# Kernel tuning notes

Hardware: AMD Instinct MI355X
Metric: run time of the kernel (lower is better)

Reference implementation:

```python
import jax, jax.numpy as jnp
import numpy as np


def setup_inputs() -> dict:
    key = jax.random.key(0)
    ks = jax.random.split(key, 7)
    B, S, E, H, D = 4, 2048, 1024, 16, 64
    return {
        "q": jax.random.normal(ks[0], (B, S, E), dtype=jnp.float32),
        "k": jax.random.normal(ks[1], (B, S, E), dtype=jnp.float32),
        "v": jax.random.normal(ks[2], (B, S, E), dtype=jnp.float32),
        "Wq": jax.random.uniform(ks[3], (H, E, D), dtype=jnp.float32),
        "Wk": jax.random.uniform(ks[4], (H, E, D), dtype=jnp.float32),
        "Wv": jax.random.uniform(ks[5], (H, E, D), dtype=jnp.float32),
        "Wo": jax.random.uniform(ks[6], (H * D, E), dtype=jnp.float32),
    }


def reference(q, k, v, Wq, Wk, Wv, Wo):
    B, S, E = q.shape
    H, _, D = Wq.shape
    qh = jnp.einsum("bse,hed->bhsd", q, Wq)
    kh = jnp.einsum("bse,hed->bhsd", k, Wk)
    vh = jnp.einsum("bse,hed->bhsd", v, Wv)
    # Faithful quirk: original divides by C**(-0.5) -> multiplies by sqrt(D)
    scale = jnp.asarray(D, q.dtype) ** 0.5
    scores = jnp.einsum("bhsd,bhtd->bhst", qh, kh) * scale  # [B,H,S,S]
    causal = jnp.tril(jnp.ones((S, S), dtype=bool))
    scores = jnp.where(causal, scores, -jnp.inf)
    attn = jax.nn.softmax(scores, axis=-1)
    out_h = jnp.einsum("bhst,bhtd->bhsd", attn, vh)  # [B,H,S,D]
    concat = out_h.transpose(0, 2, 1, 3).reshape(B, S, H * D)
    return concat @ Wo
```

## Files before the change

### kernel.cpp

```cpp
#include <hip/hip_runtime.h>
#include <hip/hip_bf16.h>

#define B_ 4
#define S_ 2048
#define E_ 1024
#define H_ 16
#define D_ 64
#define LDW 40

typedef _Float16 f16;
typedef __attribute__((ext_vector_type(4))) float f32x4;
typedef __attribute__((ext_vector_type(8))) short bf16x8;
typedef __attribute__((ext_vector_type(8))) unsigned short u16x8;
typedef __attribute__((ext_vector_type(8))) _Float16 f16x8;
typedef __attribute__((ext_vector_type(4))) float float4v;

__device__ __forceinline__ unsigned short f2bf(float f) {
  union { float f; unsigned int u; } x; x.f = f;
  unsigned int u = x.u;
  u = (u + 0x7FFFu + ((u >> 16) & 1u)) >> 16;
  return (unsigned short)u;
}

#define MFMA_BF(a, b, c) __builtin_amdgcn_mfma_f32_16x16x32_bf16((a), (b), (c), 0, 0, 0)
#define MFMA_F16(a, b, c) __builtin_amdgcn_mfma_f32_16x16x32_f16((a), (b), (c), 0, 0, 0)

__global__ __launch_bounds__(256)
void transpose_convert(const float* __restrict__ src, unsigned short* __restrict__ dst,
                       int R, int C, float scale) {
  __shared__ unsigned short tile[64][65];
  const int rb = blockIdx.y * 64;
  const int cb = blockIdx.x * 64;
  const size_t mo = (size_t)blockIdx.z * (size_t)R * (size_t)C;
  const int t = threadIdx.x;
  const int r = t >> 2;
  const int c0 = (t & 3) * 16;
  const float* sp = src + mo + (size_t)(rb + r) * C + cb + c0;
#pragma unroll
  for (int j = 0; j < 16; j += 4) {
    float4v vv = *(const float4v*)(sp + j);
    tile[r][c0 + j + 0] = f2bf(vv[0] * scale);
    tile[r][c0 + j + 1] = f2bf(vv[1] * scale);
    tile[r][c0 + j + 2] = f2bf(vv[2] * scale);
    tile[r][c0 + j + 3] = f2bf(vv[3] * scale);
  }
  __syncthreads();
  u16x8 w0, w1;
#pragma unroll
  for (int j = 0; j < 8; ++j) w0[j] = tile[c0 + j][r];
#pragma unroll
  for (int j = 0; j < 8; ++j) w1[j] = tile[c0 + 8 + j][r];
  unsigned short* dp = dst + mo + (size_t)(cb + r) * R + rb + c0;
  *(u16x8*)(dp) = w0;
  *(u16x8*)(dp + 8) = w1;
}

__global__ __launch_bounds__(256)
void transpose_split_f16(const float* __restrict__ src, f16* __restrict__ dhi,
                         f16* __restrict__ dlo, int R, int C, float scale) {
  __shared__ float tile[64][65];
  const int rb = blockIdx.y * 64;
  const int cb = blockIdx.x * 64;
  const size_t mo = (size_t)blockIdx.z * (size_t)R * (size_t)C;
  const int t = threadIdx.x;
  const int r = t >> 2;
  const int c0 = (t & 3) * 16;
  const float* sp = src + mo + (size_t)(rb + r) * C + cb + c0;
#pragma unroll
  for (int j = 0; j < 16; j += 4) {
    float4v vv = *(const float4v*)(sp + j);
    tile[r][c0 + j + 0] = vv[0] * scale;
    tile[r][c0 + j + 1] = vv[1] * scale;
    tile[r][c0 + j + 2] = vv[2] * scale;
    tile[r][c0 + j + 3] = vv[3] * scale;
  }
  __syncthreads();
  f16x8 h0, h1, l0, l1;
#pragma unroll
  for (int j = 0; j < 8; ++j) {
    float x = tile[c0 + j][r];
    f16 hi = (f16)x;
    h0[j] = hi; l0[j] = (f16)(x - (float)hi);
  }
#pragma unroll
  for (int j = 0; j < 8; ++j) {
    float x = tile[c0 + 8 + j][r];
    f16 hi = (f16)x;
    h1[j] = hi; l1[j] = (f16)(x - (float)hi);
  }
  const size_t o = mo + (size_t)(cb + r) * R + rb + c0;
  *(f16x8*)(dhi + o) = h0; *(f16x8*)(dhi + o + 8) = h1;
  *(f16x8*)(dlo + o) = l0; *(f16x8*)(dlo + o + 8) = l1;
}

__global__ __launch_bounds__(256)
void prep_split(const float* __restrict__ x, f16* __restrict__ xh, f16* __restrict__ xl) {
  const size_t i = ((size_t)blockIdx.x * 256 + threadIdx.x) * 8;
  float4v a = *(const float4v*)(x + i);
  float4v b = *(const float4v*)(x + i + 4);
  f16x8 h, lo;
#pragma unroll
  for (int j = 0; j < 4; ++j) {
    f16 hi = (f16)a[j]; h[j] = hi; lo[j] = (f16)(a[j] - (float)hi);
  }
#pragma unroll
  for (int j = 0; j < 4; ++j) {
    f16 hi = (f16)b[j]; h[4 + j] = hi; lo[4 + j] = (f16)(b[j] - (float)hi);
  }
  *(f16x8*)(xh + i) = h;
  *(f16x8*)(xl + i) = lo;
}

__global__ __launch_bounds__(256)
void prep_bf16(const float* __restrict__ x, unsigned short* __restrict__ xo) {
  const size_t i = ((size_t)blockIdx.x * 256 + threadIdx.x) * 8;
  float4v a = *(const float4v*)(x + i);
  float4v b = *(const float4v*)(x + i + 4);
  u16x8 o;
#pragma unroll
  for (int j = 0; j < 4; ++j) { o[j] = f2bf(a[j]); o[4 + j] = f2bf(b[j]); }
  *(u16x8*)(xo + i) = o;
}

__global__ __launch_bounds__(256, 2)
void proj_qk2(const f16* __restrict__ xh, const f16* __restrict__ xl,
              const f16* __restrict__ Wh, const f16* __restrict__ Wl,
              f16* __restrict__ out_hi, f16* __restrict__ out_lo) {
  __shared__ f16 Ah[128 * LDW], Al[128 * LDW], Bh[128 * LDW], Bl[128 * LDW];
  const int t = threadIdx.x;
  const int m0 = blockIdx.x * 128, n0 = blockIdx.y * 128;
  const int w = t >> 6, l = t & 63, lr = l & 15, lg = l >> 4;
  const int wm = (w & 1) * 64, wn = (w >> 1) * 64;

  const int sr0 = t >> 2, sc = (t & 3) * 8;
  const f16* gAh = xh + (size_t)(m0 + sr0) * 1024 + sc;
  const f16* gAl = xl + (size_t)(m0 + sr0) * 1024 + sc;
  const f16* gBh = Wh + (size_t)(n0 + sr0) * 1024 + sc;
  const f16* gBl = Wl + (size_t)(n0 + sr0) * 1024 + sc;
  const size_t rstep = (size_t)64 * 1024;
  const int l0 = sr0 * LDW + sc, l1 = (sr0 + 64) * LDW + sc;

  f32x4 acc[4][4];
#pragma unroll
  for (int im = 0; im < 4; ++im)
#pragma unroll
    for (int in = 0; in < 4; ++in) acc[im][in] = (f32x4){0.f, 0.f, 0.f, 0.f};

  f16x8 r0 = *(const f16x8*)(gAh),         r1 = *(const f16x8*)(gAh + rstep);
  f16x8 r2 = *(const f16x8*)(gAl),         r3 = *(const f16x8*)(gAl + rstep);
  f16x8 r4 = *(const f16x8*)(gBh),         r5 = *(const f16x8*)(gBh + rstep);
  f16x8 r6 = *(const f16x8*)(gBl),         r7 = *(const f16x8*)(gBl + rstep);
  *(f16x8*)&Ah[l0] = r0; *(f16x8*)&Ah[l1] = r1;
  *(f16x8*)&Al[l0] = r2; *(f16x8*)&Al[l1] = r3;
  *(f16x8*)&Bh[l0] = r4; *(f16x8*)&Bh[l1] = r5;
  *(f16x8*)&Bl[l0] = r6; *(f16x8*)&Bl[l1] = r7;

  for (int k0 = 0; k0 < 1024; k0 += 32) {
    __syncthreads();
    const bool pf = (k0 + 32 < 1024);
    if (pf) {
      r0 = *(const f16x8*)(gAh + k0 + 32); r1 = *(const f16x8*)(gAh + rstep + k0 + 32);
      r2 = *(const f16x8*)(gAl + k0 + 32); r3 = *(const f16x8*)(gAl + rstep + k0 + 32);
      r4 = *(const f16x8*)(gBh + k0 + 32); r5 = *(const f16x8*)(gBh + rstep + k0 + 32);
      r6 = *(const f16x8*)(gBl + k0 + 32); r7 = *(const f16x8*)(gBl + rstep + k0 + 32);
    }
    f16x8 afh[4], afl[4], bfh[4], bfl[4];
#pragma unroll
    for (int im = 0; im < 4; ++im) {
      afh[im] = *(const f16x8*)&Ah[(wm + im * 16 + lr) * LDW + lg * 8];
      afl[im] = *(const f16x8*)&Al[(wm + im * 16 + lr) * LDW + lg * 8];
    }
#pragma unroll
    for (int in = 0; in < 4; ++in) {
      bfh[in] = *(const f16x8*)&Bh[(wn + in * 16 + lr) * LDW + lg * 8];
      bfl[in] = *(const f16x8*)&Bl[(wn + in * 16 + lr) * LDW + lg * 8];
    }
#pragma unroll
    for (int im = 0; im < 4; ++im)
#pragma unroll
      for (int in = 0; in < 4; ++in) {
        acc[im][in] = MFMA_F16(afh[im], bfh[in], acc[im][in]);
        acc[im][in] = MFMA_F16(afh[im], bfl[in], acc[im][in]);
        acc[im][in] = MFMA_F16(afl[im], bfh[in], acc[im][in]);
      }
    __syncthreads();
    if (pf) {
      *(f16x8*)&Ah[l0] = r0; *(f16x8*)&Ah[l1] = r1;
      *(f16x8*)&Al[l0] = r2; *(f16x8*)&Al[l1] = r3;
      *(f16x8*)&Bh[l0] = r4; *(f16x8*)&Bh[l1] = r5;
      *(f16x8*)&Bl[l0] = r6; *(f16x8*)&Bl[l1] = r7;
    }
  }

  const int b = m0 >> 11, s0b = m0 & 2047;
#pragma unroll
  for (int im = 0; im < 4; ++im)
#pragma unroll
    for (int in = 0; in < 4; ++in)
#pragma unroll
      for (int rr = 0; rr < 4; ++rr) {
        const int srow = s0b + wm + im * 16 + lg * 4 + rr;
        const int n = n0 + wn + in * 16 + lr;
        const int h = n >> 6, d = n & 63;
        const size_t o = (((size_t)b * H_ + h) * S_ + srow) * D_ + d;
        const float x = acc[im][in][rr];
        const f16 hi = (f16)x;
        out_hi[o] = hi;
        out_lo[o] = (f16)(x - (float)hi);
      }
}

__global__ __launch_bounds__(256, 2)
void proj_v2(const unsigned short* __restrict__ xv, const unsigned short* __restrict__ Wv,
             f16* __restrict__ vht) {
  __shared__ short smem[17408];
  unsigned short* As = (unsigned short*)smem;
  unsigned short* Bs = As + 128 * LDW;
  const int t = threadIdx.x;
  const int m0 = blockIdx.x * 128, n0 = blockIdx.y * 128;
  const int w = t >> 6, l = t & 63, lr = l & 15, lg = l >> 4;
  const int wm = (w & 1) * 64, wn = (w >> 1) * 64;

  const int sr0 = t >> 2, sc = (t & 3) * 8;
  const unsigned short* gA = xv + (size_t)(m0 + sr0) * 1024 + sc;
  const unsigned short* gB = Wv + (size_t)(n0 + sr0) * 1024 + sc;
  const size_t rstep = (size_t)64 * 1024;
  const int l0 = sr0 * LDW + sc, l1 = (sr0 + 64) * LDW + sc;

  f32x4 acc[4][4];
#pragma unroll
  for (int im = 0; im < 4; ++im)
#pragma unroll
    for (int in = 0; in < 4; ++in) acc[im][in] = (f32x4){0.f, 0.f, 0.f, 0.f};

  u16x8 r0 = *(const u16x8*)(gA), r1 = *(const u16x8*)(gA + rstep);
  u16x8 r2 = *(const u16x8*)(gB), r3 = *(const u16x8*)(gB + rstep);
  *(u16x8*)&As[l0] = r0; *(u16x8*)&As[l1] = r1;
  *(u16x8*)&Bs[l0] = r2; *(u16x8*)&Bs[l1] = r3;

  for (int k0 = 0; k0 < 1024; k0 += 32) {
    __syncthreads();
    const bool pf = (k0 + 32 < 1024);
    if (pf) {
      r0 = *(const u16x8*)(gA + k0 + 32); r1 = *(const u16x8*)(gA + rstep + k0 + 32);
      r2 = *(const u16x8*)(gB + k0 + 32); r3 = *(const u16x8*)(gB + rstep + k0 + 32);
    }
    bf16x8 af[4], bf[4];
#pragma unroll
    for (int im = 0; im < 4; ++im)
      af[im] = *(const bf16x8*)&As[(wm + im * 16 + lr) * LDW + lg * 8];
#pragma unroll
    for (int in = 0; in < 4; ++in)
      bf[in] = *(const bf16x8*)&Bs[(wn + in * 16 + lr) * LDW + lg * 8];
#pragma unroll
    for (int im = 0; im < 4; ++im)
#pragma unroll
      for (int in = 0; in < 4; ++in)
        acc[im][in] = MFMA_BF(af[im], bf[in], acc[im][in]);
    __syncthreads();
    if (pf) {
      *(u16x8*)&As[l0] = r0; *(u16x8*)&As[l1] = r1;
      *(u16x8*)&Bs[l0] = r2; *(u16x8*)&Bs[l1] = r3;
    }
  }

  __syncthreads();
  f16* Td = (f16*)smem;
#pragma unroll
  for (int im = 0; im < 4; ++im)
#pragma unroll
    for (int in = 0; in < 4; ++in)
#pragma unroll
      for (int rr = 0; rr < 4; ++rr) {
        const int srow = wm + im * 16 + lg * 4 + rr;
        const int ncol = wn + in * 16 + lr;
        Td[ncol * 136 + srow] = (f16)acc[im][in][rr];
      }
  __syncthreads();
  const int n = t >> 1, sc2 = (t & 1) * 64;
  const int b = m0 >> 11, s0b = m0 & 2047;
  const int h = (n0 + n) >> 6, d = (n0 + n) & 63;
  f16* vp = vht + (((size_t)b * H_ + h) * D_ + d) * S_ + s0b + sc2;
#pragma unroll
  for (int j = 0; j < 8; ++j)
    *(f16x8*)(vp + j * 8) = *(const f16x8*)&Td[n * 136 + sc2 + j * 8];
}

__global__ __launch_bounds__(256, 2)
void out_gemm2(const unsigned short* __restrict__ A, const unsigned short* __restrict__ Bt,
               float* __restrict__ Cout) {
  __shared__ unsigned short As[128 * LDW], Bs[128 * LDW];
  const int t = threadIdx.x;
  const int m0 = blockIdx.x * 128, n0 = blockIdx.y * 128;
  const int w = t >> 6, l = t & 63, lr = l & 15, lg = l >> 4;
  const int wm = (w & 1) * 64, wn = (w >> 1) * 64;

  const int sr0 = t >> 2, sc = (t & 3) * 8;
  const unsigned short* gA = A + (size_t)(m0 + sr0) * 1024 + sc;
  const unsigned short* gB = Bt + (size_t)(n0 + sr0) * 1024 + sc;
  const size_t rstep = (size_t)64 * 1024;
  const int l0 = sr0 * LDW + sc, l1 = (sr0 + 64) * LDW + sc;

  f32x4 acc[4][4];
#pragma unroll
  for (int im = 0; im < 4; ++im)
#pragma unroll
    for (int in = 0; in < 4; ++in) acc[im][in] = (f32x4){0.f, 0.f, 0.f, 0.f};

  u16x8 r0 = *(const u16x8*)(gA), r1 = *(const u16x8*)(gA + rstep);
  u16x8 r2 = *(const u16x8*)(gB), r3 = *(const u16x8*)(gB + rstep);
  *(u16x8*)&As[l0] = r0; *(u16x8*)&As[l1] = r1;
  *(u16x8*)&Bs[l0] = r2; *(u16x8*)&Bs[l1] = r3;

  for (int k0 = 0; k0 < 1024; k0 += 32) {
    __syncthreads();
    const bool pf = (k0 + 32 < 1024);
    if (pf) {
      r0 = *(const u16x8*)(gA + k0 + 32); r1 = *(const u16x8*)(gA + rstep + k0 + 32);
      r2 = *(const u16x8*)(gB + k0 + 32); r3 = *(const u16x8*)(gB + rstep + k0 + 32);
    }
    bf16x8 af[4], bf[4];
#pragma unroll
    for (int im = 0; im < 4; ++im)
      af[im] = *(const bf16x8*)&As[(wm + im * 16 + lr) * LDW + lg * 8];
#pragma unroll
    for (int in = 0; in < 4; ++in)
      bf[in] = *(const bf16x8*)&Bs[(wn + in * 16 + lr) * LDW + lg * 8];
#pragma unroll
    for (int im = 0; im < 4; ++im)
#pragma unroll
      for (int in = 0; in < 4; ++in)
        acc[im][in] = MFMA_BF(af[im], bf[in], acc[im][in]);
    __syncthreads();
    if (pf) {
      *(u16x8*)&As[l0] = r0; *(u16x8*)&As[l1] = r1;
      *(u16x8*)&Bs[l0] = r2; *(u16x8*)&Bs[l1] = r3;
    }
  }

#pragma unroll
  for (int im = 0; im < 4; ++im)
#pragma unroll
    for (int in = 0; in < 4; ++in)
#pragma unroll
      for (int rr = 0; rr < 4; ++rr) {
        const int row = m0 + wm + im * 16 + lg * 4 + rr;
        const int col = n0 + wn + in * 16 + lr;
        Cout[(size_t)row * 1024 + col] = acc[im][in][rr];
      }
}

__global__ __launch_bounds__(256, 2)
void attn_kernel(const f16* __restrict__ qhh, const f16* __restrict__ qhl,
                 const f16* __restrict__ khh, const f16* __restrict__ khl,
                 const f16* __restrict__ vht, unsigned short* __restrict__ ao) {
  __shared__ f16 Ksh[2][64 * 64];
  __shared__ f16 Ksl[2][64 * 64];
  __shared__ f16 Vts[2][64 * 64];
  __shared__ f16 Pls[4][32 * 64];
  const int t = threadIdx.x;
  const int b = blockIdx.z, h = blockIdx.y;
  const int w = t >> 6, l = t & 63, lr = l & 15, lg = l >> 4;
  const size_t bh = ((size_t)b * H_ + h) * S_;
  const size_t bhD = ((size_t)b * H_ + h) * D_;
  const int cr0 = t >> 3, cch = t & 7;
  const int cr1 = (t + 256) >> 3;
  const int coff = (cch * 16);

#pragma unroll
  for (int ph = 0; ph < 2; ++ph) {
    const int qt = ph ? (15 - (int)blockIdx.x) : (int)blockIdx.x;
    const int q0 = qt * 128;

    f16x8 qfh[2][2], qfl[2][2];
#pragma unroll
    for (int i = 0; i < 2; ++i) {
      const size_t qo = (bh + q0 + w * 32 + i * 16 + lr) * D_;
#pragma unroll
      for (int hf = 0; hf < 2; ++hf) {
        qfh[i][hf] = *(const f16x8*)(qhh + qo + hf * 32 + lg * 8);
        qfl[i][hf] = *(const f16x8*)(qhl + qo + hf * 32 + lg * 8);
      }
    }

    f32x4 acc[2][4];
#pragma unroll
    for (int i = 0; i < 2; ++i)
#pragma unroll
      for (int c = 0; c < 4; ++c) acc[i][c] = (f32x4){0.f, 0.f, 0.f, 0.f};
    float mx[2][4], ls[2][4];
#pragma unroll
    for (int i = 0; i < 2; ++i)
#pragma unroll
      for (int r = 0; r < 4; ++r) { mx[i][r] = -3.0e38f; ls[i][r] = 0.f; }

    const int wmax = q0 + w * 32 + 31;
    const int nkt = 2 * qt + 2;
    int cur = 0;

    {
      const f16* kbh = khh + bh * D_;
      const f16* kbl = khl + bh * D_;
      const f16* vb = vht + bhD * S_;
      f16x8 a0 = *(const f16x8*)(kbh + cr0 * 64 + cch * 8);
      f16x8 a1 = *(const f16x8*)(kbh + cr1 * 64 + cch * 8);
      f16x8 b0 = *(const f16x8*)(kbl + cr0 * 64 + cch * 8);
      f16x8 b1 = *(const f16x8*)(kbl + cr1 * 64 + cch * 8);
      f16x8 c0 = *(const f16x8*)(vb + (size_t)cr0 * S_ + cch * 8);
      f16x8 c1 = *(const f16x8*)(vb + (size_t)cr1 * S_ + cch * 8);
      const int o0 = coff ^ ((cr0 & 7) << 4);
      const int o1 = coff ^ ((cr1 & 7) << 4);
      *(f16x8*)((char*)Ksh[0] + cr0 * 128 + o0) = a0;
      *(f16x8*)((char*)Ksh[0] + cr1 * 128 + o1) = a1;
      *(f16x8*)((char*)Ksl[0] + cr0 * 128 + o0) = b0;
      *(f16x8*)((char*)Ksl[0] + cr1 * 128 + o1) = b1;
      *(f16x8*)((char*)Vts[0] + cr0 * 128 + o0) = c0;
      *(f16x8*)((char*)Vts[0] + cr1 * 128 + o1) = c1;
    }

    for (int kt = 0; kt < nkt; ++kt) {
      const int kt0 = kt * 64;
      __syncthreads();

      const bool pf = (kt + 1 < nkt);
      f16x8 ra0, ra1, rb0, rb1, rc0, rc1;
      if (pf) {
        const int n0 = kt0 + 64;
        const f16* kbh = khh + (bh + n0) * D_;
        const f16* kbl = khl + (bh + n0) * D_;
        const f16* vb = vht + bhD * S_ + n0;
        ra0 = *(const f16x8*)(kbh + cr0 * 64 + cch * 8);
        ra1 = *(const f16x8*)(kbh + cr1 * 64 + cch * 8);
        rb0 = *(const f16x8*)(kbl + cr0 * 64 + cch * 8);
        rb1 = *(const f16x8*)(kbl + cr1 * 64 + cch * 8);
        rc0 = *(const f16x8*)(vb + (size_t)cr0 * S_ + cch * 8);
        rc1 = *(const f16x8*)(vb + (size_t)cr1 * S_ + cch * 8);
      }

      if (kt0 <= wmax) {
        f32x4 sc[2][4];
#pragma unroll
        for (int n = 0; n < 4; ++n) {
          const int krow = n * 16 + lr;
          const int sw = (krow & 7) << 4;
          const char* kb = (const char*)Ksh[cur] + krow * 128;
          const char* kbl2 = (const char*)Ksl[cur] + krow * 128;
          f16x8 kh0 = *(const f16x8*)(kb + ((lg * 16) ^ sw));
          f16x8 kh1 = *(const f16x8*)(kb + ((64 + lg * 16) ^ sw));
          f16x8 kl0 = *(const f16x8*)(kbl2 + ((lg * 16) ^ sw));
          f16x8 kl1 = *(const f16x8*)(kbl2 + ((64 + lg * 16) ^ sw));
#pragma unroll
          for (int i = 0; i < 2; ++i) {
            f32x4 z = (f32x4){0.f, 0.f, 0.f, 0.f};
            z = MFMA_F16(qfh[i][0], kh0, z);
            z = MFMA_F16(qfh[i][1], kh1, z);
            z = MFMA_F16(qfh[i][0], kl0, z);
            z = MFMA_F16(qfh[i][1], kl1, z);
            z = MFMA_F16(qfl[i][0], kh0, z);
            z = MFMA_F16(qfl[i][1], kh1, z);
            sc[i][n] = z;
          }
        }

#pragma unroll
        for (int i = 0; i < 2; ++i) {
          const int qbase = q0 + w * 32 + i * 16;
          const bool full = (kt0 + 63 <= qbase);
#pragma unroll
          for (int r = 0; r < 4; ++r) {
            const int qrow = qbase + lg * 4 + r;
            float v0 = sc[i][0][r], v1 = sc[i][1][r], v2 = sc[i][2][r], v3 = sc[i][3][r];
            if (!full) {
              v0 = (kt0 + 0 + lr <= qrow) ? v0 : -3.0e38f;
              v1 = (kt0 + 16 + lr <= qrow) ? v1 : -3.0e38f;
              v2 = (kt0 + 32 + lr <= qrow) ? v2 : -3.0e38f;
              v3 = (kt0 + 48 + lr <= qrow) ? v3 : -3.0e38f;
            }
            float tm = fmaxf(fmaxf(v0, v1), fmaxf(v2, v3));
            tm = fmaxf(tm, __shfl_xor(tm, 1));
            tm = fmaxf(tm, __shfl_xor(tm, 2));
            tm = fmaxf(tm, __shfl_xor(tm, 4));
            tm = fmaxf(tm, __shfl_xor(tm, 8));
            const float mn = fmaxf(mx[i][r], tm);
            const float corr = __expf(mx[i][r] - mn);
            mx[i][r] = mn;
            float p0 = __expf(v0 - mn), p1 = __expf(v1 - mn);
            float p2 = __expf(v2 - mn), p3 = __expf(v3 - mn);
            float ps = (p0 + p1) + (p2 + p3);
            ps += __shfl_xor(ps, 1);
            ps += __shfl_xor(ps, 2);
            ps += __shfl_xor(ps, 4);
            ps += __shfl_xor(ps, 8);
            ls[i][r] = ls[i][r] * corr + ps;
#pragma unroll
            for (int c = 0; c < 4; ++c) acc[i][c][r] *= corr;
            const int qi = i * 16 + lg * 4 + r;
            char* pb = (char*)&Pls[w][0] + qi * 128;
            const int sw2 = (qi & 7) << 4;
            *(f16*)(pb + ((0 + lr * 2) ^ sw2)) = (f16)p0;
            *(f16*)(pb + ((32 + lr * 2) ^ sw2)) = (f16)p1;
            *(f16*)(pb + ((64 + lr * 2) ^ sw2)) = (f16)p2;
            *(f16*)(pb + ((96 + lr * 2) ^ sw2)) = (f16)p3;
          }
        }

#pragma unroll
        for (int ks = 0; ks < 2; ++ks) {
          const int co = (ks * 64 + lg * 16);
          f16x8 pf0 = *(const f16x8*)((const char*)&Pls[w][0] + lr * 128 + (co ^ ((lr & 7) << 4)));
          f16x8 pf1 = *(const f16x8*)((const char*)&Pls[w][0] + (16 + lr) * 128 + (co ^ ((lr & 7) << 4)));
#pragma unroll
          for (int c = 0; c < 4; ++c) {
            const int vr = c * 16 + lr;
            f16x8 vf = *(const f16x8*)((const char*)Vts[cur] + vr * 128 + (co ^ ((vr & 7) << 4)));
            acc[0][c] = MFMA_F16(pf0, vf, acc[0][c]);
            acc[1][c] = MFMA_F16(pf1, vf, acc[1][c]);
          }
        }
      }

      __syncthreads();
      if (pf) {
        const int nb = cur ^ 1;
        const int o0 = coff ^ ((cr0 & 7) << 4);
        const int o1 = coff ^ ((cr1 & 7) << 4);
        *(f16x8*)((char*)Ksh[nb] + cr0 * 128 + o0) = ra0;
        *(f16x8*)((char*)Ksh[nb] + cr1 * 128 + o1) = ra1;
        *(f16x8*)((char*)Ksl[nb] + cr0 * 128 + o0) = rb0;
        *(f16x8*)((char*)Ksl[nb] + cr1 * 128 + o1) = rb1;
        *(f16x8*)((char*)Vts[nb] + cr0 * 128 + o0) = rc0;
        *(f16x8*)((char*)Vts[nb] + cr1 * 128 + o1) = rc1;
      }
      cur ^= 1;
    }

#pragma unroll
    for (int i = 0; i < 2; ++i)
#pragma unroll
      for (int r = 0; r < 4; ++r) {
        const float inv = 1.0f / ls[i][r];
        const size_t s = q0 + w * 32 + i * 16 + lg * 4 + r;
        const size_t o = ((size_t)b * S_ + s) * (H_ * D_) + (size_t)h * D_;
#pragma unroll
        for (int c = 0; c < 4; ++c)
          ao[o + c * 16 + lr] = f2bf(acc[i][c][r] * inv);
      }
  }
}

extern "C" void kernel_launch(void* const* d_in, const int* in_sizes, int n_in,
                              void* d_out, int out_size, void* d_ws, size_t ws_size,
                              hipStream_t stream) {
  const float* q = (const float*)d_in[0];
  const float* k = (const float*)d_in[1];
  const float* v = (const float*)d_in[2];
  const float* Wq = (const float*)d_in[3];
  const float* Wk = (const float*)d_in[4];
  const float* Wv = (const float*)d_in[5];
  const float* Wo = (const float*)d_in[6];

  const size_t NBH = (size_t)B_ * H_ * S_ * D_;
  const size_t WSZ = (size_t)H_ * D_ * E_;

  char* wsb = (char*)d_ws;
  f16* Wqk_hi = (f16*)wsb;
  f16* Wqk_lo = Wqk_hi + 2 * WSZ;
  unsigned short* Wvt = (unsigned short*)(Wqk_lo + 2 * WSZ);
  unsigned short* Wot = Wvt + WSZ;
  f16* qk_hi = (f16*)(wsb + (size_t)12 * 1024 * 1024);
  f16* qk_lo = qk_hi + 2 * NBH;
  char* flex = wsb + (size_t)76 * 1024 * 1024;
  f16* xh = (f16*)flex;
  f16* xl = (f16*)(flex + (size_t)16 * 1024 * 1024);
  unsigned short* xv = (unsigned short*)flex;
  f16* vht = (f16*)(flex + (size_t)16 * 1024 * 1024);
  unsigned short* ao = (unsigned short*)flex;

  dim3 blk(256);
  transpose_split_f16<<<dim3(1, 16, 16), blk, 0, stream>>>(Wq, Wqk_hi, Wqk_lo, E_, D_, 8.0f);
  transpose_split_f16<<<dim3(1, 16, 16), blk, 0, stream>>>(Wk, Wqk_hi + WSZ, Wqk_lo + WSZ, E_, D_, 1.0f);
  transpose_convert<<<dim3(1, 16, 16), blk, 0, stream>>>(Wv, Wvt, E_, D_, 1.0f);
  transpose_convert<<<dim3(16, 16, 1), blk, 0, stream>>>(Wo, Wot, E_, E_, 1.0f);
  prep_split<<<dim3(4096), blk, 0, stream>>>(q, xh, xl);
  proj_qk2<<<dim3(64, 8), blk, 0, stream>>>(xh, xl, Wqk_hi, Wqk_lo, qk_hi, qk_lo);
  prep_split<<<dim3(4096), blk, 0, stream>>>(k, xh, xl);
  proj_qk2<<<dim3(64, 8), blk, 0, stream>>>(xh, xl, Wqk_hi + WSZ, Wqk_lo + WSZ,
                                            qk_hi + NBH, qk_lo + NBH);
  prep_bf16<<<dim3(4096), blk, 0, stream>>>(v, xv);
  proj_v2<<<dim3(64, 8), blk, 0, stream>>>(xv, Wvt, vht);
  attn_kernel<<<dim3(S_ / 256, H_, B_), blk, 0, stream>>>(
      qk_hi, qk_lo, qk_hi + NBH, qk_lo + NBH, vht, ao);
  out_gemm2<<<dim3(64, 8), blk, 0, stream>>>(ao, Wot, (float*)d_out);
}
```

Before: 498.7 us.

## Load GEMM tiles directly from global memory into LDS with global_load_lds

Replaces the register-staged global-to-shared copies in the Q/K, V and output projection GEMMs with the global_load_lds builtin, which writes 16-byte chunks straight into LDS. The LDS tiles lose their padding (row stride 40 becomes 32) so each wave's contiguous lane writes map onto the tile layout. The aim is to cut VGPR pressure and the extra LDS store instructions. In exchange it drops the register prefetch that overlapped the next tile's global loads with the current tile's MFMAs, and the unpadded stride may cause LDS bank conflicts on fragment reads.

```diff
diff --git a/kernel.cpp b/kernel.cpp
--- a/kernel.cpp
+++ b/kernel.cpp
@@ -6,7 +6,6 @@
 #define E_ 1024
 #define H_ 16
 #define D_ 64
-#define LDW 40
 
 typedef _Float16 f16;
 typedef __attribute__((ext_vector_type(4))) float f32x4;
@@ -24,6 +23,10 @@
 
 #define MFMA_BF(a, b, c) __builtin_amdgcn_mfma_f32_16x16x32_bf16((a), (b), (c), 0, 0, 0)
 #define MFMA_F16(a, b, c) __builtin_amdgcn_mfma_f32_16x16x32_f16((a), (b), (c), 0, 0, 0)
+
+#define GLDS16(g, s) __builtin_amdgcn_global_load_lds( \
+    (const __attribute__((address_space(1))) void*)(g), \
+    (__attribute__((address_space(3))) void*)(s), 16, 0, 0)
 
 __global__ __launch_bounds__(256)
 void transpose_convert(const float* __restrict__ src, unsigned short* __restrict__ dst,
@@ -123,22 +126,16 @@
 }
 
 __global__ __launch_bounds__(256, 2)
-void proj_qk2(const f16* __restrict__ xh, const f16* __restrict__ xl,
+void proj_qk3(const f16* __restrict__ xh, const f16* __restrict__ xl,
               const f16* __restrict__ Wh, const f16* __restrict__ Wl,
               f16* __restrict__ out_hi, f16* __restrict__ out_lo) {
-  __shared__ f16 Ah[128 * LDW], Al[128 * LDW], Bh[128 * LDW], Bl[128 * LDW];
+  __shared__ f16 Ah[128 * 32], Al[128 * 32], Bh[128 * 32], Bl[128 * 32];
   const int t = threadIdx.x;
   const int m0 = blockIdx.x * 128, n0 = blockIdx.y * 128;
   const int w = t >> 6, l = t & 63, lr = l & 15, lg = l >> 4;
   const int wm = (w & 1) * 64, wn = (w >> 1) * 64;
-
-  const int sr0 = t >> 2, sc = (t & 3) * 8;
-  const f16* gAh = xh + (size_t)(m0 + sr0) * 1024 + sc;
-  const f16* gAl = xl + (size_t)(m0 + sr0) * 1024 + sc;
-  const f16* gBh = Wh + (size_t)(n0 + sr0) * 1024 + sc;
-  const f16* gBl = Wl + (size_t)(n0 + sr0) * 1024 + sc;
-  const size_t rstep = (size_t)64 * 1024;
-  const int l0 = sr0 * LDW + sc, l1 = (sr0 + 64) * LDW + sc;
+  const int srow = w * 32 + (l >> 2);
+  const int scol = (l & 3) * 8;
 
   f32x4 acc[4][4];
 #pragma unroll
@@ -146,34 +143,29 @@
 #pragma unroll
     for (int in = 0; in < 4; ++in) acc[im][in] = (f32x4){0.f, 0.f, 0.f, 0.f};
 
-  f16x8 r0 = *(const f16x8*)(gAh),         r1 = *(const f16x8*)(gAh + rstep);
-  f16x8 r2 = *(const f16x8*)(gAl),         r3 = *(const f16x8*)(gAl + rstep);
-  f16x8 r4 = *(const f16x8*)(gBh),         r5 = *(const f16x8*)(gBh + rstep);
-  f16x8 r6 = *(const f16x8*)(gBl),         r7 = *(const f16x8*)(gBl + rstep);
-  *(f16x8*)&Ah[l0] = r0; *(f16x8*)&Ah[l1] = r1;
-  *(f16x8*)&Al[l0] = r2; *(f16x8*)&Al[l1] = r3;
-  *(f16x8*)&Bh[l0] = r4; *(f16x8*)&Bh[l1] = r5;
-  *(f16x8*)&Bl[l0] = r6; *(f16x8*)&Bl[l1] = r7;
-
   for (int k0 = 0; k0 < 1024; k0 += 32) {
+#pragma unroll
+    for (int j = 0; j < 2; ++j) {
+      const size_t ga = (size_t)(m0 + srow + j * 16) * 1024 + scol + k0;
+      const size_t gb = (size_t)(n0 + srow + j * 16) * 1024 + scol + k0;
+      const int lo = (w * 32 + j * 16) * 32;
+      GLDS16(xh + ga, &Ah[lo]);
+      GLDS16(xl + ga, &Al[lo]);
+      GLDS16(Wh + gb, &Bh[lo]);
+      GLDS16(Wl + gb, &Bl[lo]);
+    }
     __syncthreads();
-    const bool pf = (k0 + 32 < 1024);
-    if (pf) {
-      r0 = *(const f16x8*)(gAh + k0 + 32); r1 = *(const f16x8*)(gAh + rstep + k0 + 32);
-      r2 = *(const f16x8*)(gAl + k0 + 32); r3 = *(const f16x8*)(gAl + rstep + k0 + 32);
-      r4 = *(const f16x8*)(gBh + k0 + 32); r5 = *(const f16x8*)(gBh + rstep + k0 + 32);
-      r6 = *(const f16x8*)(gBl + k0 + 32); r7 = *(const f16x8*)(gBl + rstep + k0 + 32);
-    }
+
     f16x8 afh[4], afl[4], bfh[4], bfl[4];
 #pragma unroll
     for (int im = 0; im < 4; ++im) {
-      afh[im] = *(const f16x8*)&Ah[(wm + im * 16 + lr) * LDW + lg * 8];
-      afl[im] = *(const f16x8*)&Al[(wm + im * 16 + lr) * LDW + lg * 8];
+      afh[im] = *(const f16x8*)&Ah[(wm + im * 16 + lr) * 32 + lg * 8];
+      afl[im] = *(const f16x8*)&Al[(wm + im * 16 + lr) * 32 + lg * 8];
     }
 #pragma unroll
     for (int in = 0; in < 4; ++in) {
-      bfh[in] = *(const f16x8*)&Bh[(wn + in * 16 + lr) * LDW + lg * 8];
-      bfl[in] = *(const f16x8*)&Bl[(wn + in * 16 + lr) * LDW + lg * 8];
+      bfh[in] = *(const f16x8*)&Bh[(wn + in * 16 + lr) * 32 + lg * 8];
+      bfl[in] = *(const f16x8*)&Bl[(wn + in * 16 + lr) * 32 + lg * 8];
     }
 #pragma unroll
     for (int im = 0; im < 4; ++im)
@@ -184,12 +176,6 @@
         acc[im][in] = MFMA_F16(afl[im], bfh[in], acc[im][in]);
       }
     __syncthreads();
-    if (pf) {
-      *(f16x8*)&Ah[l0] = r0; *(f16x8*)&Ah[l1] = r1;
-      *(f16x8*)&Al[l0] = r2; *(f16x8*)&Al[l1] = r3;
-      *(f16x8*)&Bh[l0] = r4; *(f16x8*)&Bh[l1] = r5;
-      *(f16x8*)&Bl[l0] = r6; *(f16x8*)&Bl[l1] = r7;
-    }
   }
 
   const int b = m0 >> 11, s0b = m0 & 2047;
@@ -199,10 +185,10 @@
     for (int in = 0; in < 4; ++in)
 #pragma unroll
       for (int rr = 0; rr < 4; ++rr) {
-        const int srow = s0b + wm + im * 16 + lg * 4 + rr;
+        const int srw = s0b + wm + im * 16 + lg * 4 + rr;
         const int n = n0 + wn + in * 16 + lr;
         const int h = n >> 6, d = n & 63;
-        const size_t o = (((size_t)b * H_ + h) * S_ + srow) * D_ + d;
+        const size_t o = (((size_t)b * H_ + h) * S_ + srw) * D_ + d;
         const float x = acc[im][in][rr];
         const f16 hi = (f16)x;
         out_hi[o] = hi;
@@ -211,21 +197,17 @@
 }
 
 __global__ __launch_bounds__(256, 2)
-void proj_v2(const unsigned short* __restrict__ xv, const unsigned short* __restrict__ Wv,
+void proj_v3(const unsigned short* __restrict__ xv, const unsigned short* __restrict__ Wv,
              f16* __restrict__ vht) {
   __shared__ short smem[17408];
   unsigned short* As = (unsigned short*)smem;
-  unsigned short* Bs = As + 128 * LDW;
+  unsigned short* Bs = As + 128 * 32;
   const int t = threadIdx.x;
   const int m0 = blockIdx.x * 128, n0 = blockIdx.y * 128;
   const int w = t >> 6, l = t & 63, lr = l & 15, lg = l >> 4;
   const int wm = (w & 1) * 64, wn = (w >> 1) * 64;
-
-  const int sr0 = t >> 2, sc = (t & 3) * 8;
-  const unsigned short* gA = xv + (size_t)(m0 + sr0) * 1024 + sc;
-  const unsigned short* gB = Wv + (size_t)(n0 + sr0) * 1024 + sc;
-  const size_t rstep = (size_t)64 * 1024;
-  const int l0 = sr0 * LDW + sc, l1 = (sr0 + 64) * LDW + sc;
+  const int srow = w * 32 + (l >> 2);
+  const int scol = (l & 3) * 8;
 
   f32x4 acc[4][4];
 #pragma unroll
@@ -233,38 +215,32 @@
 #pragma unroll
     for (int in = 0; in < 4; ++in) acc[im][in] = (f32x4){0.f, 0.f, 0.f, 0.f};
 
-  u16x8 r0 = *(const u16x8*)(gA), r1 = *(const u16x8*)(gA + rstep);
-  u16x8 r2 = *(const u16x8*)(gB), r3 = *(const u16x8*)(gB + rstep);
-  *(u16x8*)&As[l0] = r0; *(u16x8*)&As[l1] = r1;
-  *(u16x8*)&Bs[l0] = r2; *(u16x8*)&Bs[l1] = r3;
-
   for (int k0 = 0; k0 < 1024; k0 += 32) {
+#pragma unroll
+    for (int j = 0; j < 2; ++j) {
+      const size_t ga = (size_t)(m0 + srow + j * 16) * 1024 + scol + k0;
+      const size_t gb = (size_t)(n0 + srow + j * 16) * 1024 + scol + k0;
+      const int lo = (w * 32 + j * 16) * 32;
+      GLDS16(xv + ga, &As[lo]);
+      GLDS16(Wv + gb, &Bs[lo]);
+    }
     __syncthreads();
-    const bool pf = (k0 + 32 < 1024);
-    if (pf) {
-      r0 = *(const u16x8*)(gA + k0 + 32); r1 = *(const u16x8*)(gA + rstep + k0 + 32);
-      r2 = *(const u16x8*)(gB + k0 + 32); r3 = *(const u16x8*)(gB + rstep + k0 + 32);
-    }
+
     bf16x8 af[4], bf[4];
 #pragma unroll
     for (int im = 0; im < 4; ++im)
-      af[im] = *(const bf16x8*)&As[(wm + im * 16 + lr) * LDW + lg * 8];
+      af[im] = *(const bf16x8*)&As[(wm + im * 16 + lr) * 32 + lg * 8];
 #pragma unroll
     for (int in = 0; in < 4; ++in)
-      bf[in] = *(const bf16x8*)&Bs[(wn + in * 16 + lr) * LDW + lg * 8];
+      bf[in] = *(const bf16x8*)&Bs[(wn + in * 16 + lr) * 32 + lg * 8];
 #pragma unroll
     for (int im = 0; im < 4; ++im)
 #pragma unroll
       for (int in = 0; in < 4; ++in)
         acc[im][in] = MFMA_BF(af[im], bf[in], acc[im][in]);
     __syncthreads();
-    if (pf) {
-      *(u16x8*)&As[l0] = r0; *(u16x8*)&As[l1] = r1;
-      *(u16x8*)&Bs[l0] = r2; *(u16x8*)&Bs[l1] = r3;
-    }
-  }
-
-  __syncthreads();
+  }
+
   f16* Td = (f16*)smem;
 #pragma unroll
   for (int im = 0; im < 4; ++im)
@@ -272,9 +248,9 @@
     for (int in = 0; in < 4; ++in)
 #pragma unroll
       for (int rr = 0; rr < 4; ++rr) {
-        const int srow = wm + im * 16 + lg * 4 + rr;
+        const int srw = wm + im * 16 + lg * 4 + rr;
         const int ncol = wn + in * 16 + lr;
-        Td[ncol * 136 + srow] = (f16)acc[im][in][rr];
+        Td[ncol * 136 + srw] = (f16)acc[im][in][rr];
       }
   __syncthreads();
   const int n = t >> 1, sc2 = (t & 1) * 64;
@@ -287,19 +263,15 @@
 }
 
 __global__ __launch_bounds__(256, 2)
-void out_gemm2(const unsigned short* __restrict__ A, const unsigned short* __restrict__ Bt,
+void out_gemm3(const unsigned short* __restrict__ A, const unsigned short* __restrict__ Bt,
                float* __restrict__ Cout) {
-  __shared__ unsigned short As[128 * LDW], Bs[128 * LDW];
+  __shared__ unsigned short As[128 * 32], Bs[128 * 32];
   const int t = threadIdx.x;
   const int m0 = blockIdx.x * 128, n0 = blockIdx.y * 128;
   const int w = t >> 6, l = t & 63, lr = l & 15, lg = l >> 4;
   const int wm = (w & 1) * 64, wn = (w >> 1) * 64;
-
-  const int sr0 = t >> 2, sc = (t & 3) * 8;
-  const unsigned short* gA = A + (size_t)(m0 + sr0) * 1024 + sc;
-  const unsigned short* gB = Bt + (size_t)(n0 + sr0) * 1024 + sc;
-  const size_t rstep = (size_t)64 * 1024;
-  const int l0 = sr0 * LDW + sc, l1 = (sr0 + 64) * LDW + sc;
+  const int srow = w * 32 + (l >> 2);
+  const int scol = (l & 3) * 8;
 
   f32x4 acc[4][4];
 #pragma unroll
@@ -307,35 +279,30 @@
 #pragma unroll
     for (int in = 0; in < 4; ++in) acc[im][in] = (f32x4){0.f, 0.f, 0.f, 0.f};
 
-  u16x8 r0 = *(const u16x8*)(gA), r1 = *(const u16x8*)(gA + rstep);
-  u16x8 r2 = *(const u16x8*)(gB), r3 = *(const u16x8*)(gB + rstep);
-  *(u16x8*)&As[l0] = r0; *(u16x8*)&As[l1] = r1;
-  *(u16x8*)&Bs[l0] = r2; *(u16x8*)&Bs[l1] = r3;
-
   for (int k0 = 0; k0 < 1024; k0 += 32) {
+#pragma unroll
+    for (int j = 0; j < 2; ++j) {
+      const size_t ga = (size_t)(m0 + srow + j * 16) * 1024 + scol + k0;
+      const size_t gb = (size_t)(n0 + srow + j * 16) * 1024 + scol + k0;
+      const int lo = (w * 32 + j * 16) * 32;
+      GLDS16(A + ga, &As[lo]);
+      GLDS16(Bt + gb, &Bs[lo]);
+    }
     __syncthreads();
-    const bool pf = (k0 + 32 < 1024);
-    if (pf) {
-      r0 = *(const u16x8*)(gA + k0 + 32); r1 = *(const u16x8*)(gA + rstep + k0 + 32);
-      r2 = *(const u16x8*)(gB + k0 + 32); r3 = *(const u16x8*)(gB + rstep + k0 + 32);
-    }
+
     bf16x8 af[4], bf[4];
 #pragma unroll
     for (int im = 0; im < 4; ++im)
-      af[im] = *(const bf16x8*)&As[(wm + im * 16 + lr) * LDW + lg * 8];
+      af[im] = *(const bf16x8*)&As[(wm + im * 16 + lr) * 32 + lg * 8];
 #pragma unroll
     for (int in = 0; in < 4; ++in)
-      bf[in] = *(const bf16x8*)&Bs[(wn + in * 16 + lr) * LDW + lg * 8];
+      bf[in] = *(const bf16x8*)&Bs[(wn + in * 16 + lr) * 32 + lg * 8];
 #pragma unroll
     for (int im = 0; im < 4; ++im)
 #pragma unroll
       for (int in = 0; in < 4; ++in)
         acc[im][in] = MFMA_BF(af[im], bf[in], acc[im][in]);
     __syncthreads();
-    if (pf) {
-      *(u16x8*)&As[l0] = r0; *(u16x8*)&As[l1] = r1;
-      *(u16x8*)&Bs[l0] = r2; *(u16x8*)&Bs[l1] = r3;
-    }
   }
 
 #pragma unroll
@@ -582,13 +549,13 @@
   transpose_convert<<<dim3(1, 16, 16), blk, 0, stream>>>(Wv, Wvt, E_, D_, 1.0f);
   transpose_convert<<<dim3(16, 16, 1), blk, 0, stream>>>(Wo, Wot, E_, E_, 1.0f);
   prep_split<<<dim3(4096), blk, 0, stream>>>(q, xh, xl);
-  proj_qk2<<<dim3(64, 8), blk, 0, stream>>>(xh, xl, Wqk_hi, Wqk_lo, qk_hi, qk_lo);
+  proj_qk3<<<dim3(64, 8), blk, 0, stream>>>(xh, xl, Wqk_hi, Wqk_lo, qk_hi, qk_lo);
   prep_split<<<dim3(4096), blk, 0, stream>>>(k, xh, xl);
-  proj_qk2<<<dim3(64, 8), blk, 0, stream>>>(xh, xl, Wqk_hi + WSZ, Wqk_lo + WSZ,
+  proj_qk3<<<dim3(64, 8), blk, 0, stream>>>(xh, xl, Wqk_hi + WSZ, Wqk_lo + WSZ,
                                             qk_hi + NBH, qk_lo + NBH);
   prep_bf16<<<dim3(4096), blk, 0, stream>>>(v, xv);
-  proj_v2<<<dim3(64, 8), blk, 0, stream>>>(xv, Wvt, vht);
+  proj_v3<<<dim3(64, 8), blk, 0, stream>>>(xv, Wvt, vht);
   attn_kernel<<<dim3(S_ / 256, H_, B_), blk, 0, stream>>>(
       qk_hi, qk_lo, qk_hi + NBH, qk_lo + NBH, vht, ao);
-  out_gemm2<<<dim3(64, 8), blk, 0, stream>>>(ao, Wot, (float*)d_out);
-}
+  out_gemm3<<<dim3(64, 8), blk, 0, stream>>>(ao, Wot, (float*)d_out);
+}
```

New measurement: 485.9 us. 2.6% less time.
